# Kernel optimization log

Measured on AMD Instinct MI355X. Metric: run time of the kernel, lower is better.

Reference implementation:

```python
import jax, jax.numpy as jnp
import numpy as np

B, L, WIN = 65536, 240, 24
EMB_SZS = [(367, 20), (7, 4), (24, 8)]
N_CONT = 16
H1, H2, OUT_SZ = 512, 256, 24
N_EMB = sum(nf for _, nf in EMB_SZS)
NUM_WAVE = 6 * (WIN // 2) + 6 * (WIN // 4)  # 108


def pool_matrix(lin, w):
    # PyTorch AdaptiveAvgPool1d: bin i averages x[floor(i*lin/w) : ceil((i+1)*lin/w)]
    P = np.zeros((lin, w), np.float32)
    for i in range(w):
        s = (i * lin) // w
        e = -((-(i + 1) * lin) // w)
        P[s:e, i] = 1.0 / (e - s)
    return jnp.asarray(P)


def conv1(x, w, dil):
    # single-channel 1D cross-correlation, no bias; x: [B, Lin], w: [ks]
    ks = w.shape[0]
    lout = x.shape[-1] - dil * (ks - 1)
    return sum(w[k] * x[:, k * dil:k * dil + lout] for k in range(ks))


def branch(xw, wa, wb):
    # conv(ks, dil=1) -> adaptive_avg_pool(12) -> leaky_relu(0.1), then same with dil=2 -> pool(6)
    ca = conv1(xw, wa, 1)                                   # [B, L-ks+1]
    fa = jax.nn.leaky_relu(ca @ pool_matrix(ca.shape[-1], WIN // 2), 0.1)  # [B,12]
    cb = conv1(fa, wb, 2)                                   # [B, 12-2*(ks-1)]
    fb = jax.nn.leaky_relu(cb @ pool_matrix(cb.shape[-1], WIN // 4), 0.1)  # [B,6]
    return fa, fb


def setup_inputs() -> dict:
    key = jax.random.key(0)
    ks_list = list(range(1, 7))
    keys = jax.random.split(key, 32)
    d = {}
    d['x_window'] = jax.random.normal(keys[0], (B, 1, L), jnp.float32)
    cats = [jax.random.randint(jax.random.fold_in(keys[1], i), (B,), 0, ni)
            for i, (ni, _) in enumerate(EMB_SZS)]
    d['x_cat'] = jnp.stack(cats, axis=1).astype(jnp.int64)
    d['x_cont'] = jax.random.normal(keys[2], (B, N_CONT), jnp.float32)
    for i, ks in enumerate(ks_list):
        d[f'wk{ks}a'] = jax.random.normal(keys[3 + 2 * i], (ks,), jnp.float32) * 0.5
        d[f'wk{ks}b'] = jax.random.normal(keys[4 + 2 * i], (ks,), jnp.float32) * 0.5
    for i, (ni, nf) in enumerate(EMB_SZS):
        d[f'E{i}'] = jax.random.normal(keys[16 + i], (ni, nf), jnp.float32) * 0.01
    d['bn_g'] = jnp.ones((N_CONT,), jnp.float32)
    d['bn_b'] = jnp.zeros((N_CONT,), jnp.float32)
    n_in = N_EMB + N_CONT
    d['W1'] = jax.random.normal(keys[20], (n_in, H1), jnp.float32) * (1.0 / np.sqrt(n_in))
    d['b1'] = jnp.zeros((H1,), jnp.float32)
    d['W2'] = jax.random.normal(keys[21], (H1, H2), jnp.float32) * (1.0 / np.sqrt(H1))
    d['b2'] = jnp.zeros((H2,), jnp.float32)
    d['Wlin'] = jax.random.normal(keys[22], (NUM_WAVE + H2, OUT_SZ), jnp.float32) * (1.0 / np.sqrt(NUM_WAVE + H2))
    return d


def reference(x_window, x_cat, x_cont,
              wk1a, wk1b, wk2a, wk2b, wk3a, wk3b, wk4a, wk4b, wk5a, wk5b, wk6a, wk6b,
              E0, E1, E2, bn_g, bn_b, W1, b1, W2, b2, Wlin):
    xw = x_window[:, 0, :]  # [B, L]
    feats = []
    for wa, wb in [(wk1a, wk1b), (wk2a, wk2b), (wk3a, wk3b),
                   (wk4a, wk4b), (wk5a, wk5b), (wk6a, wk6b)]:
        fa, fb = branch(xw, wa, wb)
        feats += [fa, fb]
    ffc = jnp.concatenate(feats, axis=1)  # [B, 108]
    # embeddings
    emb = jnp.concatenate([E0[x_cat[:, 0]], E1[x_cat[:, 1]], E2[x_cat[:, 2]]], axis=1)  # [B, 32]
    # BatchNorm1d on continuous features (training-mode batch stats, eps=1e-5)
    m = jnp.mean(x_cont, axis=0)
    v = jnp.var(x_cont, axis=0)
    xc = (x_cont - m) / jnp.sqrt(v + 1e-5) * bn_g + bn_b
    x = jnp.concatenate([emb, xc], axis=1)  # [B, 48]
    x = jax.nn.relu(x @ W1 + b1)
    x = jax.nn.relu(x @ W2 + b2)  # [B, 256]
    fc = jnp.concatenate([ffc, x], axis=1)  # [B, 364]
    return fc @ Wlin  # [B, 24]
```

## Files before the change

### kernel.cpp

```cpp
#include <hip/hip_runtime.h>

typedef __bf16 bf16x8 __attribute__((ext_vector_type(8)));
typedef float  f32x4  __attribute__((ext_vector_type(4)));
typedef unsigned short ushort_t;

#define B_TOTAL 65536

__device__ __forceinline__ ushort_t f2bf(float f) {
  unsigned u = __builtin_bit_cast(unsigned, f);
  u += 0x7fffu + ((u >> 16) & 1u);
  return (ushort_t)(u >> 16);
}
__device__ __forceinline__ unsigned pk2(float lo, float hi) {
  unsigned r;
  asm("v_cvt_pk_bf16_f32 %0, %1, %2" : "=v"(r) : "v"(lo), "v"(hi));
  return r;
}
__device__ __forceinline__ float lrelu(float v) { return v >= 0.f ? v : 0.1f * v; }
__device__ __forceinline__ bf16x8 ld_frag(const ushort_t* p8) {
  return __builtin_bit_cast(bf16x8, *(const uint4*)p8);
}
__device__ __forceinline__ bf16x8 ld_tile(const ushort_t* base, int tile, int lane) {
  return __builtin_bit_cast(bf16x8,
      *(const uint4*)((const char*)base + tile * 1024 + lane * 16));
}
__device__ __forceinline__ char* frag_addr4(ushort_t* base, int k, int s15, int st) {
  int kb = k >> 5, g = (k >> 3) & 3, i = k & 7;
  return (char*)base + (((kb * 4 + st) * 64) + s15 + g * 16) * 16 + i * 2;
}
__device__ __forceinline__ f32x4 mfma16(bf16x8 a, bf16x8 b, f32x4 c) {
  return __builtin_amdgcn_mfma_f32_16x16x32_bf16(a, b, c, 0, 0, 0);
}

__global__ __launch_bounds__(256) void bn_partial(const float* __restrict__ xc,
                                                  float* __restrict__ ws) {
  __shared__ float red[512];
  const int t = threadIdx.x;
  const int c = t & 15, g = t >> 4;
  const int r0 = blockIdx.x * 256;
  float s = 0.f, q = 0.f;
  for (int i = 0; i < 16; ++i) {
    float v = xc[(size_t)(r0 + g + i * 16) * 16 + c];
    s += v; q += v * v;
  }
  red[t] = s; red[256 + t] = q;
  __syncthreads();
  if (t < 16) {
    float ss = 0.f, qq = 0.f;
    for (int gg = 0; gg < 16; ++gg) { ss += red[gg * 16 + t]; qq += red[256 + gg * 16 + t]; }
    ws[blockIdx.x * 32 + t] = ss;
    ws[blockIdx.x * 32 + 16 + t] = qq;
  }
}

__global__ __launch_bounds__(256) void bn_final(const float* __restrict__ ws_in,
                                                float* __restrict__ ws_out,
                                                const float* __restrict__ g_,
                                                const float* __restrict__ b_) {
  __shared__ float red[512];
  const int t = threadIdx.x;
  const int c = t & 15, g = t >> 4;
  float s = 0.f, q = 0.f;
  for (int i = 0; i < 16; ++i) {
    int blk = g * 16 + i;
    s += ws_in[blk * 32 + c];
    q += ws_in[blk * 32 + 16 + c];
  }
  red[t] = s; red[256 + t] = q;
  __syncthreads();
  if (t < 16) {
    float ss = 0.f, qq = 0.f;
    for (int gg = 0; gg < 16; ++gg) { ss += red[gg * 16 + t]; qq += red[256 + gg * 16 + t]; }
    float mean  = ss / (float)B_TOTAL;
    float var   = qq / (float)B_TOTAL - mean * mean;
    float scale = g_[t] / sqrtf(var + 1e-5f);
    ws_out[8192 + t]      = scale;
    ws_out[8192 + 16 + t] = b_[t] - mean * scale;
  }
}

__global__ __launch_bounds__(256) void pack_weights(const float* __restrict__ W1,
                                                    const float* __restrict__ W2,
                                                    const float* __restrict__ Wl,
                                                    ushort_t* __restrict__ w1p,
                                                    ushort_t* __restrict__ w2p,
                                                    ushort_t* __restrict__ wlp) {
  int u = blockIdx.x * 256 + threadIdx.x;
  if (u < 32768) {
    int i = u & 7, lane = (u >> 3) & 63, kb = u >> 14;
    int k = kb * 32 + ((lane >> 4) << 3) + i;
    int n = (((u >> 9) & 31) << 4) + (lane & 15);
    w1p[u] = f2bf(k < 48 ? W1[k * 512 + n] : 0.f);
  } else if (u < 32768 + 131072) {
    int v = u - 32768;
    int i = v & 7, lane = (v >> 3) & 63, kb = v >> 13;
    int k = kb * 32 + ((lane >> 4) << 3) + i;
    int n = (((v >> 9) & 15) << 4) + (lane & 15);
    w2p[v] = f2bf(W2[k * 256 + n]);
  } else if (u < 32768 + 131072 + 12288) {
    int v = u - (32768 + 131072);
    int i = v & 7, lane = (v >> 3) & 63, kb = v >> 10;
    int k = kb * 32 + ((lane >> 4) << 3) + i;
    int n = (((v >> 9) & 1) << 4) + (lane & 15);
    float val = 0.f;
    if (n < 24) {
      if (k < 108)       val = Wl[k * 24 + n];
      else if (k >= 128) val = Wl[(k - 20) * 24 + n];
    }
    wlp[v] = f2bf(val);
  }
}

struct WkPtrs { const float* wk[12]; };

__global__ __launch_bounds__(256) void pack_conv(WkPtrs wp,
                                                 ushort_t* __restrict__ Apack,
                                                 ushort_t* __restrict__ Bpack) {
  int u = blockIdx.x * 256 + threadIdx.x;
  if (u < 20480) {
    int i = u & 7, lane = (u >> 3) & 63;
    int knt = u >> 9;
    int kb = knt / 5, nt = knt % 5;
    int k = kb * 32 + ((lane >> 4) << 3) + i;
    int n = nt * 16 + (lane & 15);
    float val = 0.f;
    if (n < 72 && k < 240) {
      int br = n / 12, ii = n - br * 12, ks = br + 1, lin = 240 - br;
      int si = ii * lin / 12, ei = ((ii + 1) * lin + 11) / 12;
      const float* wa = wp.wk[2 * br];
      float acc = 0.f;
      for (int kk = 0; kk < ks; ++kk) {
        int j = k - kk;
        if (j >= si && j < ei) acc += wa[kk];
      }
      val = acc / (float)(ei - si);
    }
    Apack[u] = f2bf(val);
  } else if (u < 20480 + 6144) {
    int v = u - 20480;
    int i = v & 7, lane = (v >> 3) & 63;
    int knt = v >> 9;
    int kb = knt / 3, nt = knt % 3;
    int kcol = kb * 32 + ((lane >> 4) << 3) + i;
    int n = nt * 16 + (lane & 15);
    float val = 0.f;
    if (n < 36 && kcol < 108) {
      int brk = kcol / 18, ii = kcol - brk * 18;
      int brn = n / 6, j = n - brn * 6;
      if (brk == brn && ii < 12) {
        int ks = brn + 1, lcb = 12 - 2 * brn;
        int sj = j * lcb / 6, ej = ((j + 1) * lcb + 5) / 6;
        const float* wb = wp.wk[2 * brn + 1];
        float acc = 0.f;
        for (int kk = 0; kk < ks; ++kk) {
          int q = ii - 2 * kk;
          if (q >= sj && q < ej) acc += wb[kk];
        }
        val = acc / (float)(ej - sj);
      }
    }
    Bpack[v] = f2bf(val);
  }
}

struct FusedParams {
  const float* xw;
  const int*   xcat;
  const float* xcont;
  const float* E0; const float* E1; const float* E2;
  const float* b1; const float* b2;
  const ushort_t* Apack; const ushort_t* Bpack;
  const ushort_t* w1p; const ushort_t* w2p; const ushort_t* wlp;
  const float* stats;
  float*       out;
};

__global__ __launch_bounds__(512, 4) void fused_kernel(FusedParams p) {
  __shared__ __align__(16) char smem[57344];
  ushort_t* s_xw  = (ushort_t*)smem;
  ushort_t* s_h1  = (ushort_t*)smem;
  ushort_t* s_h2  = (ushort_t*)smem;
  ushort_t* s_cf  = (ushort_t*)(smem + 32768);
  ushort_t* s_x48 = (ushort_t*)(smem + 49152);

  const int t    = threadIdx.x;
  const int lane = t & 63;
  const int w    = t >> 6;
  const int quad = lane >> 4;
  const int s15  = lane & 15;
  const int s0   = blockIdx.x * 64;
  const f32x4 fzero = {0.f, 0.f, 0.f, 0.f};

  ((uint4*)s_cf)[t] = uint4{0, 0, 0, 0};
  ((uint4*)s_cf)[t + 512] = uint4{0, 0, 0, 0};
  if (t < 128) {
    *(uint4*)((char*)s_xw + (28 + (t >> 5)) * 1024 + 512 + (t & 31) * 16) = uint4{0, 0, 0, 0};
  } else if (t < 256) {
    int tt = t - 128;
    *(uint4*)((char*)s_x48 + (4 + (tt >> 5)) * 1024 + 512 + (tt & 31) * 16) = uint4{0, 0, 0, 0};
  }
  for (int u = t; u < 64 * 60; u += 512) {
    int s = u / 60, m4 = u - s * 60;
    float4 v = *(const float4*)(p.xw + (size_t)(s0 + s) * 240 + 4 * m4);
    uint2 pkv; pkv.x = pk2(v.x, v.y); pkv.y = pk2(v.z, v.w);
    int tile = (m4 >> 3) * 4 + (s >> 4);
    *(uint2*)((char*)s_xw + (tile * 64 + (s & 15) + ((m4 >> 1) & 3) * 16) * 16
              + (m4 & 1) * 8) = pkv;
  }
  for (int u = t; u < 64 * 48; u += 512) {
    int s = u / 48, c = u - s * 48, gs = s0 + s;
    float v;
    if (c < 20)      v = p.E0[(size_t)p.xcat[gs * 3 + 0] * 20 + c];
    else if (c < 24) v = p.E1[(size_t)p.xcat[gs * 3 + 1] * 4 + (c - 20)];
    else if (c < 32) v = p.E2[(size_t)p.xcat[gs * 3 + 2] * 8 + (c - 24)];
    else { int cc = c - 32; v = p.xcont[(size_t)gs * 16 + cc] * p.stats[cc] + p.stats[16 + cc]; }
    *(ushort_t*)frag_addr4(s_x48, c, s & 15, s >> 4) = f2bf(v);
  }
  __syncthreads();

  auto do0a = [&](int nt, int st) {
    f32x4 acc = fzero;
    #pragma unroll
    for (int kb = 0; kb < 8; ++kb) {
      bf16x8 a = ld_frag(p.Apack + (size_t)((kb * 5 + nt) * 64 + lane) * 8);
      bf16x8 b = ld_tile(s_xw, kb * 4 + st, lane);
      acc = mfma16(a, b, acc);
    }
    int n0 = nt * 16 + quad * 4;
    int br = n0 / 12;
    int col0 = n0 + 6 * br;
    *(unsigned*)frag_addr4(s_cf, col0, s15, st)     = pk2(lrelu(acc[0]), lrelu(acc[1]));
    *(unsigned*)frag_addr4(s_cf, col0 + 2, s15, st) = pk2(lrelu(acc[2]), lrelu(acc[3]));
  };
  do0a(w % 5, w / 5);
  do0a((w + 8) % 5, (w + 8) / 5);
  if (w < 4) do0a((w + 16) % 5, (w + 16) / 5);
  __syncthreads();

  const int nt2 = w * 2;
  uint4 pa[2][2];
  #pragma unroll
  for (int q = 0; q < 2; ++q) {
    pa[q][0] = *(const uint4*)(p.w2p + (size_t)((q * 16 + nt2 + 0) * 64 + lane) * 8);
    pa[q][1] = *(const uint4*)(p.w2p + (size_t)((q * 16 + nt2 + 1) * 64 + lane) * 8);
  }

  const int ntB0 = w % 3,       stB0 = w / 3;
  const int ntB1 = (w + 8) % 3, stB1 = (w + 8) / 3;
  f32x4 accB0 = fzero, accB1 = fzero;
  #pragma unroll
  for (int kb = 0; kb < 4; ++kb) {
    bf16x8 a = ld_frag(p.Bpack + (size_t)((kb * 3 + ntB0) * 64 + lane) * 8);
    bf16x8 b = ld_tile(s_cf, kb * 4 + stB0, lane);
    accB0 = mfma16(a, b, accB0);
  }
  if (w < 4) {
    #pragma unroll
    for (int kb = 0; kb < 4; ++kb) {
      bf16x8 a = ld_frag(p.Bpack + (size_t)((kb * 3 + ntB1) * 64 + lane) * 8);
      bf16x8 b = ld_tile(s_cf, kb * 4 + stB1, lane);
      accB1 = mfma16(a, b, accB1);
    }
  }

  auto gemm1_half = [&](int h) {
    #pragma unroll
    for (int j = 0; j < 2; ++j) {
      int ntp = w * 2 + j;
      int gnt = h * 16 + ntp;
      bf16x8 a0 = ld_frag(p.w1p + (size_t)((0 * 32 + gnt) * 64 + lane) * 8);
      bf16x8 a1 = ld_frag(p.w1p + (size_t)((32 + gnt) * 64 + lane) * 8);
      f32x4 acc[4];
      #pragma unroll
      for (int st = 0; st < 4; ++st) {
        bf16x8 b0 = ld_tile(s_x48, 0 * 4 + st, lane);
        bf16x8 b1 = ld_tile(s_x48, 1 * 4 + st, lane);
        acc[st] = mfma16(a0, b0, fzero);
        acc[st] = mfma16(a1, b1, acc[st]);
      }
      int n0l = ntp * 16 + quad * 4;
      float4 bb = *(const float4*)(p.b1 + h * 256 + n0l);
      int kb1 = ntp >> 1;
      int g   = (ntp * 2 + (quad >> 1)) & 3;
      #pragma unroll
      for (int st = 0; st < 4; ++st) {
        float v0 = fmaxf(acc[st][0] + bb.x, 0.f);
        float v1 = fmaxf(acc[st][1] + bb.y, 0.f);
        float v2 = fmaxf(acc[st][2] + bb.z, 0.f);
        float v3 = fmaxf(acc[st][3] + bb.w, 0.f);
        uint2 pkv; pkv.x = pk2(v0, v1); pkv.y = pk2(v2, v3);
        *(uint2*)((char*)s_h1 + ((kb1 * 4 + st) * 64 + s15 + g * 16) * 16
                  + (quad & 1) * 8) = pkv;
      }
    }
  };
  gemm1_half(0);
  __syncthreads();

  auto wr0b = [&](f32x4 acc, int nt, int st) {
    int n0 = nt * 16 + quad * 4;
    if (n0 < 36) {
      int br0 = n0 / 6, c0 = n0 + 12 * (br0 + 1);
      int n2 = n0 + 2, br2 = n2 / 6, c2 = n2 + 12 * (br2 + 1);
      *(unsigned*)frag_addr4(s_cf, c0, s15, st) = pk2(lrelu(acc[0]), lrelu(acc[1]));
      *(unsigned*)frag_addr4(s_cf, c2, s15, st) = pk2(lrelu(acc[2]), lrelu(acc[3]));
    }
  };
  wr0b(accB0, ntB0, stB0);
  if (w < 4) wr0b(accB1, ntB1, stB1);

  f32x4 acc2[2][4];
  #pragma unroll
  for (int jm = 0; jm < 2; ++jm)
    #pragma unroll
    for (int st = 0; st < 4; ++st) acc2[jm][st] = fzero;

  auto gemm2_half = [&](int k0) {
    #pragma unroll
    for (int kk = 0; kk < 8; ++kk) {
      int kb = k0 + kk;
      bf16x8 a0 = __builtin_bit_cast(bf16x8, pa[kb & 1][0]);
      bf16x8 a1 = __builtin_bit_cast(bf16x8, pa[kb & 1][1]);
      if (kb + 2 < 16) {
        pa[kb & 1][0] = *(const uint4*)(p.w2p + (size_t)(((kb + 2) * 16 + nt2 + 0) * 64 + lane) * 8);
        pa[kb & 1][1] = *(const uint4*)(p.w2p + (size_t)(((kb + 2) * 16 + nt2 + 1) * 64 + lane) * 8);
      }
      #pragma unroll
      for (int st = 0; st < 4; ++st) {
        bf16x8 b = ld_tile(s_h1, kk * 4 + st, lane);
        acc2[0][st] = mfma16(a0, b, acc2[0][st]);
        acc2[1][st] = mfma16(a1, b, acc2[1][st]);
      }
    }
  };
  gemm2_half(0);
  __syncthreads();

  gemm1_half(1);
  __syncthreads();

  gemm2_half(8);
  __syncthreads();

  #pragma unroll
  for (int jm = 0; jm < 2; ++jm) {
    int n0 = (nt2 + jm) * 16 + quad * 4;
    float4 bb = *(const float4*)(p.b2 + n0);
    int kbh = (nt2 + jm) >> 1;
    int g   = ((nt2 + jm) * 2 + (quad >> 1)) & 3;
    #pragma unroll
    for (int st = 0; st < 4; ++st) {
      float v0 = fmaxf(acc2[jm][st][0] + bb.x, 0.f);
      float v1 = fmaxf(acc2[jm][st][1] + bb.y, 0.f);
      float v2 = fmaxf(acc2[jm][st][2] + bb.z, 0.f);
      float v3 = fmaxf(acc2[jm][st][3] + bb.w, 0.f);
      uint2 pkv; pkv.x = pk2(v0, v1); pkv.y = pk2(v2, v3);
      *(uint2*)((char*)s_h2 + ((kbh * 4 + st) * 64 + s15 + g * 16) * 16
                + (quad & 1) * 8) = pkv;
    }
  }
  __syncthreads();

  {
    const int st = w & 3, nt = w >> 2;
    f32x4 acc = fzero;
    #pragma unroll
    for (int kb = 0; kb < 12; ++kb) {
      bf16x8 a = ld_frag(p.wlp + (size_t)((kb * 2 + nt) * 64 + lane) * 8);
      bf16x8 b = (kb < 4) ? ld_tile(s_cf, kb * 4 + st, lane)
                          : ld_tile(s_h2, (kb - 4) * 4 + st, lane);
      acc = mfma16(a, b, acc);
    }
    int n0 = nt * 16 + quad * 4;
    if (n0 < 24) {
      int sg = s0 + st * 16 + s15;
      *(float2*)(p.out + (size_t)sg * 24 + n0)     = make_float2(acc[0], acc[1]);
      *(float2*)(p.out + (size_t)sg * 24 + n0 + 2) = make_float2(acc[2], acc[3]);
    }
  }
}

extern "C" void kernel_launch(void* const* d_in, const int* in_sizes, int n_in,
                              void* d_out, int out_size, void* d_ws, size_t ws_size,
                              hipStream_t stream) {
  const float* xcont = (const float*)d_in[2];
  float* ws  = (float*)d_ws;
  char*  wsb = (char*)d_ws;
  ushort_t* w1p   = (ushort_t*)(wsb + 36864);
  ushort_t* w2p   = (ushort_t*)(wsb + 102400);
  ushort_t* wlp   = (ushort_t*)(wsb + 364544);
  ushort_t* Apack = (ushort_t*)(wsb + 389120);
  ushort_t* Bpack = (ushort_t*)(wsb + 430080);

  WkPtrs wp;
  for (int i = 0; i < 12; ++i) wp.wk[i] = (const float*)d_in[3 + i];
  pack_conv<<<104, 256, 0, stream>>>(wp, Apack, Bpack);
  bn_partial<<<256, 256, 0, stream>>>(xcont, ws);
  bn_final<<<1, 256, 0, stream>>>(ws, ws, (const float*)d_in[18], (const float*)d_in[19]);
  pack_weights<<<688, 256, 0, stream>>>((const float*)d_in[20], (const float*)d_in[22],
                                        (const float*)d_in[24], w1p, w2p, wlp);

  FusedParams p;
  p.xw    = (const float*)d_in[0];
  p.xcat  = (const int*)d_in[1];
  p.xcont = xcont;
  p.E0 = (const float*)d_in[15]; p.E1 = (const float*)d_in[16]; p.E2 = (const float*)d_in[17];
  p.b1 = (const float*)d_in[21]; p.b2 = (const float*)d_in[23];
  p.Apack = Apack; p.Bpack = Bpack;
  p.w1p = w1p; p.w2p = w2p; p.wlp = wlp;
  p.stats = ws + 8192;
  p.out = (float*)d_out;
  fused_kernel<<<B_TOTAL / 64, 512, 0, stream>>>(p);
}
```

Before: 65.67 us.

## Double block size to 1024 threads with one n-tile per wave

The fused kernel now launches 16 waves per block instead of 8. Each wave owns a single 16-column tile in the conv-pool, GEMM1, GEMM2 and final stages instead of two, so the prefetch buffers and accumulators shrink by half. The aim is to cut per-thread register use and put more waves in flight per CU, since LDS per block is unchanged, which should hide global-load and MFMA latency better. In exchange, each __syncthreads now waits on twice as many waves, and several waves sit idle in the phase-B conv and final output stages.

```diff
diff --git a/kernel.cpp b/kernel.cpp
--- a/kernel.cpp
+++ b/kernel.cpp
@@ -175,7 +175,7 @@
   float*       out;
 };
 
-__global__ __launch_bounds__(512, 4) void fused_kernel(FusedParams p) {
+__global__ __launch_bounds__(1024, 8) void fused_kernel(FusedParams p) {
   __shared__ __align__(16) char smem[57344];
   ushort_t* s_xw  = (ushort_t*)smem;
   ushort_t* s_h1  = (ushort_t*)smem;
@@ -192,14 +192,13 @@
   const f32x4 fzero = {0.f, 0.f, 0.f, 0.f};
 
   ((uint4*)s_cf)[t] = uint4{0, 0, 0, 0};
-  ((uint4*)s_cf)[t + 512] = uint4{0, 0, 0, 0};
   if (t < 128) {
     *(uint4*)((char*)s_xw + (28 + (t >> 5)) * 1024 + 512 + (t & 31) * 16) = uint4{0, 0, 0, 0};
   } else if (t < 256) {
     int tt = t - 128;
     *(uint4*)((char*)s_x48 + (4 + (tt >> 5)) * 1024 + 512 + (tt & 31) * 16) = uint4{0, 0, 0, 0};
   }
-  for (int u = t; u < 64 * 60; u += 512) {
+  for (int u = t; u < 64 * 60; u += 1024) {
     int s = u / 60, m4 = u - s * 60;
     float4 v = *(const float4*)(p.xw + (size_t)(s0 + s) * 240 + 4 * m4);
     uint2 pkv; pkv.x = pk2(v.x, v.y); pkv.y = pk2(v.z, v.w);
@@ -207,7 +206,7 @@
     *(uint2*)((char*)s_xw + (tile * 64 + (s & 15) + ((m4 >> 1) & 3) * 16) * 16
               + (m4 & 1) * 8) = pkv;
   }
-  for (int u = t; u < 64 * 48; u += 512) {
+  for (int u = t; u < 64 * 48; u += 1024) {
     int s = u / 48, c = u - s * 48, gs = s0 + s;
     float v;
     if (c < 20)      v = p.E0[(size_t)p.xcat[gs * 3 + 0] * 20 + c];
@@ -233,103 +232,81 @@
     *(unsigned*)frag_addr4(s_cf, col0 + 2, s15, st) = pk2(lrelu(acc[2]), lrelu(acc[3]));
   };
   do0a(w % 5, w / 5);
-  do0a((w + 8) % 5, (w + 8) / 5);
   if (w < 4) do0a((w + 16) % 5, (w + 16) / 5);
   __syncthreads();
 
-  const int nt2 = w * 2;
-  uint4 pa[2][2];
-  #pragma unroll
-  for (int q = 0; q < 2; ++q) {
-    pa[q][0] = *(const uint4*)(p.w2p + (size_t)((q * 16 + nt2 + 0) * 64 + lane) * 8);
-    pa[q][1] = *(const uint4*)(p.w2p + (size_t)((q * 16 + nt2 + 1) * 64 + lane) * 8);
-  }
-
-  const int ntB0 = w % 3,       stB0 = w / 3;
-  const int ntB1 = (w + 8) % 3, stB1 = (w + 8) / 3;
-  f32x4 accB0 = fzero, accB1 = fzero;
-  #pragma unroll
-  for (int kb = 0; kb < 4; ++kb) {
-    bf16x8 a = ld_frag(p.Bpack + (size_t)((kb * 3 + ntB0) * 64 + lane) * 8);
-    bf16x8 b = ld_tile(s_cf, kb * 4 + stB0, lane);
-    accB0 = mfma16(a, b, accB0);
-  }
-  if (w < 4) {
+  const int nt2 = w;
+  uint4 pa[2];
+  pa[0] = *(const uint4*)(p.w2p + (size_t)((0 * 16 + nt2) * 64 + lane) * 8);
+  pa[1] = *(const uint4*)(p.w2p + (size_t)((1 * 16 + nt2) * 64 + lane) * 8);
+
+  const int ntB = w % 3, stB = w / 3;
+  f32x4 accB = fzero;
+  if (w < 12) {
     #pragma unroll
     for (int kb = 0; kb < 4; ++kb) {
-      bf16x8 a = ld_frag(p.Bpack + (size_t)((kb * 3 + ntB1) * 64 + lane) * 8);
-      bf16x8 b = ld_tile(s_cf, kb * 4 + stB1, lane);
-      accB1 = mfma16(a, b, accB1);
+      bf16x8 a = ld_frag(p.Bpack + (size_t)((kb * 3 + ntB) * 64 + lane) * 8);
+      bf16x8 b = ld_tile(s_cf, kb * 4 + stB, lane);
+      accB = mfma16(a, b, accB);
     }
   }
 
   auto gemm1_half = [&](int h) {
-    #pragma unroll
-    for (int j = 0; j < 2; ++j) {
-      int ntp = w * 2 + j;
-      int gnt = h * 16 + ntp;
-      bf16x8 a0 = ld_frag(p.w1p + (size_t)((0 * 32 + gnt) * 64 + lane) * 8);
-      bf16x8 a1 = ld_frag(p.w1p + (size_t)((32 + gnt) * 64 + lane) * 8);
-      f32x4 acc[4];
-      #pragma unroll
-      for (int st = 0; st < 4; ++st) {
-        bf16x8 b0 = ld_tile(s_x48, 0 * 4 + st, lane);
-        bf16x8 b1 = ld_tile(s_x48, 1 * 4 + st, lane);
-        acc[st] = mfma16(a0, b0, fzero);
-        acc[st] = mfma16(a1, b1, acc[st]);
-      }
-      int n0l = ntp * 16 + quad * 4;
-      float4 bb = *(const float4*)(p.b1 + h * 256 + n0l);
-      int kb1 = ntp >> 1;
-      int g   = (ntp * 2 + (quad >> 1)) & 3;
-      #pragma unroll
-      for (int st = 0; st < 4; ++st) {
-        float v0 = fmaxf(acc[st][0] + bb.x, 0.f);
-        float v1 = fmaxf(acc[st][1] + bb.y, 0.f);
-        float v2 = fmaxf(acc[st][2] + bb.z, 0.f);
-        float v3 = fmaxf(acc[st][3] + bb.w, 0.f);
-        uint2 pkv; pkv.x = pk2(v0, v1); pkv.y = pk2(v2, v3);
-        *(uint2*)((char*)s_h1 + ((kb1 * 4 + st) * 64 + s15 + g * 16) * 16
-                  + (quad & 1) * 8) = pkv;
-      }
+    int gnt = h * 16 + w;
+    bf16x8 a0 = ld_frag(p.w1p + (size_t)((0 * 32 + gnt) * 64 + lane) * 8);
+    bf16x8 a1 = ld_frag(p.w1p + (size_t)((32 + gnt) * 64 + lane) * 8);
+    f32x4 acc[4];
+    #pragma unroll
+    for (int st = 0; st < 4; ++st) {
+      bf16x8 b0 = ld_tile(s_x48, 0 * 4 + st, lane);
+      bf16x8 b1 = ld_tile(s_x48, 1 * 4 + st, lane);
+      acc[st] = mfma16(a0, b0, fzero);
+      acc[st] = mfma16(a1, b1, acc[st]);
+    }
+    int n0l = w * 16 + quad * 4;
+    float4 bb = *(const float4*)(p.b1 + h * 256 + n0l);
+    int kb1 = w >> 1;
+    int g   = (w * 2 + (quad >> 1)) & 3;
+    #pragma unroll
+    for (int st = 0; st < 4; ++st) {
+      float v0 = fmaxf(acc[st][0] + bb.x, 0.f);
+      float v1 = fmaxf(acc[st][1] + bb.y, 0.f);
+      float v2 = fmaxf(acc[st][2] + bb.z, 0.f);
+      float v3 = fmaxf(acc[st][3] + bb.w, 0.f);
+      uint2 pkv; pkv.x = pk2(v0, v1); pkv.y = pk2(v2, v3);
+      *(uint2*)((char*)s_h1 + ((kb1 * 4 + st) * 64 + s15 + g * 16) * 16
+                + (quad & 1) * 8) = pkv;
     }
   };
   gemm1_half(0);
   __syncthreads();
 
-  auto wr0b = [&](f32x4 acc, int nt, int st) {
-    int n0 = nt * 16 + quad * 4;
+  if (w < 12) {
+    int n0 = ntB * 16 + quad * 4;
     if (n0 < 36) {
       int br0 = n0 / 6, c0 = n0 + 12 * (br0 + 1);
       int n2 = n0 + 2, br2 = n2 / 6, c2 = n2 + 12 * (br2 + 1);
-      *(unsigned*)frag_addr4(s_cf, c0, s15, st) = pk2(lrelu(acc[0]), lrelu(acc[1]));
-      *(unsigned*)frag_addr4(s_cf, c2, s15, st) = pk2(lrelu(acc[2]), lrelu(acc[3]));
-    }
-  };
-  wr0b(accB0, ntB0, stB0);
-  if (w < 4) wr0b(accB1, ntB1, stB1);
-
-  f32x4 acc2[2][4];
+      *(unsigned*)frag_addr4(s_cf, c0, s15, stB) = pk2(lrelu(accB[0]), lrelu(accB[1]));
+      *(unsigned*)frag_addr4(s_cf, c2, s15, stB) = pk2(lrelu(accB[2]), lrelu(accB[3]));
+    }
+  }
+
+  f32x4 acc2[4];
   #pragma unroll
-  for (int jm = 0; jm < 2; ++jm)
-    #pragma unroll
-    for (int st = 0; st < 4; ++st) acc2[jm][st] = fzero;
+  for (int st = 0; st < 4; ++st) acc2[st] = fzero;
 
   auto gemm2_half = [&](int k0) {
     #pragma unroll
     for (int kk = 0; kk < 8; ++kk) {
       int kb = k0 + kk;
-      bf16x8 a0 = __builtin_bit_cast(bf16x8, pa[kb & 1][0]);
-      bf16x8 a1 = __builtin_bit_cast(bf16x8, pa[kb & 1][1]);
+      bf16x8 a0 = __builtin_bit_cast(bf16x8, pa[kb & 1]);
       if (kb + 2 < 16) {
-        pa[kb & 1][0] = *(const uint4*)(p.w2p + (size_t)(((kb + 2) * 16 + nt2 + 0) * 64 + lane) * 8);
-        pa[kb & 1][1] = *(const uint4*)(p.w2p + (size_t)(((kb + 2) * 16 + nt2 + 1) * 64 + lane) * 8);
+        pa[kb & 1] = *(const uint4*)(p.w2p + (size_t)(((kb + 2) * 16 + nt2) * 64 + lane) * 8);
       }
       #pragma unroll
       for (int st = 0; st < 4; ++st) {
         bf16x8 b = ld_tile(s_h1, kk * 4 + st, lane);
-        acc2[0][st] = mfma16(a0, b, acc2[0][st]);
-        acc2[1][st] = mfma16(a1, b, acc2[1][st]);
+        acc2[st] = mfma16(a0, b, acc2[st]);
       }
     }
   };
@@ -342,18 +319,17 @@
   gemm2_half(8);
   __syncthreads();
 
-  #pragma unroll
-  for (int jm = 0; jm < 2; ++jm) {
-    int n0 = (nt2 + jm) * 16 + quad * 4;
+  {
+    int n0 = nt2 * 16 + quad * 4;
     float4 bb = *(const float4*)(p.b2 + n0);
-    int kbh = (nt2 + jm) >> 1;
-    int g   = ((nt2 + jm) * 2 + (quad >> 1)) & 3;
+    int kbh = nt2 >> 1;
+    int g   = (nt2 * 2 + (quad >> 1)) & 3;
     #pragma unroll
     for (int st = 0; st < 4; ++st) {
-      float v0 = fmaxf(acc2[jm][st][0] + bb.x, 0.f);
-      float v1 = fmaxf(acc2[jm][st][1] + bb.y, 0.f);
-      float v2 = fmaxf(acc2[jm][st][2] + bb.z, 0.f);
-      float v3 = fmaxf(acc2[jm][st][3] + bb.w, 0.f);
+      float v0 = fmaxf(acc2[st][0] + bb.x, 0.f);
+      float v1 = fmaxf(acc2[st][1] + bb.y, 0.f);
+      float v2 = fmaxf(acc2[st][2] + bb.z, 0.f);
+      float v3 = fmaxf(acc2[st][3] + bb.w, 0.f);
       uint2 pkv; pkv.x = pk2(v0, v1); pkv.y = pk2(v2, v3);
       *(uint2*)((char*)s_h2 + ((kbh * 4 + st) * 64 + s15 + g * 16) * 16
                 + (quad & 1) * 8) = pkv;
@@ -361,7 +337,7 @@
   }
   __syncthreads();
 
-  {
+  if (w < 8) {
     const int st = w & 3, nt = w >> 2;
     f32x4 acc = fzero;
     #pragma unroll
@@ -410,5 +386,5 @@
   p.w1p = w1p; p.w2p = w2p; p.wlp = wlp;
   p.stats = ws + 8192;
   p.out = (float*)d_out;
-  fused_kernel<<<B_TOTAL / 64, 512, 0, stream>>>(p);
-}
+  fused_kernel<<<B_TOTAL / 64, 1024, 0, stream>>>(p);
+}
```

Result: faster. 62.49 us (-4.8%).
